# Kernel tuning notes

Hardware: AMD Instinct MI355X
Metric: run time of the kernel (lower is better)

Reference implementation:

```python
import jax, jax.numpy as jnp
import numpy as np

GRAY = 0.2989 + 0.5870 + 0.1140  # tf.image.rgb_to_grayscale weight sum (channels identical after grayscale_to_rgb)


def _resample(img, coords, axis):
    """Bilinear 1-D resample of `img` along `axis` at float `coords` (clamped)."""
    n = img.shape[axis]
    i0f = jnp.floor(coords)
    i0 = jnp.clip(i0f, 0, n - 1).astype(jnp.int32)
    i1 = jnp.clip(i0f + 1.0, 0, n - 1).astype(jnp.int32)
    f = coords - i0f
    a = jnp.take(img, i0, axis=axis)
    b = jnp.take(img, i1, axis=axis)
    shp = [1] * img.ndim
    shp[axis] = -1
    f = f.reshape(shp)
    return a * (1.0 - f) + b * f


def _aug_one(img, off_f, b, c, size, docrop, flp, k):
    S = img.shape[0]
    # ---- random crop (prob 0.5) + bilinear resize back to SxS (half-pixel centers) ----
    size_f = jnp.where(docrop, size.astype(jnp.float32), float(S))
    off = jnp.where(docrop, jnp.floor(off_f * (S - size_f + 1.0)), 0.0)  # [2] integer-valued offsets
    idx = (jnp.arange(S, dtype=jnp.float32) + 0.5) * (size_f / S) - 0.5
    img = _resample(img, idx + off[0], 0)
    img = _resample(img, idx + off[1], 1)
    # ---- random flip_left_right + rot90(k) ----
    img = jnp.where(flp, img[:, ::-1, :], img)
    rots = jnp.stack([img,
                      jnp.rot90(img, 1, (0, 1)),
                      jnp.rot90(img, 2, (0, 1)),
                      jnp.rot90(img, 3, (0, 1))])
    img = rots[k]
    # ---- per-channel brightness + contrast (gray->rgb->gray round trip == GRAY scale) ----
    x = img + b  # [S,S,C] + [C]
    m = jnp.mean(x, axis=(0, 1), keepdims=True)
    x = (x - m) * c + m
    return x * GRAY


def setup_inputs() -> dict:
    B, S, C = 64, 256, 5
    key = jax.random.key(0)
    ks = jax.random.split(key, 8)
    crops = jax.random.normal(ks[0], (B, S, S, C), dtype=jnp.float32)
    crop_size = jax.random.randint(ks[1], (B,), int(0.8 * S), S, dtype=jnp.int32)
    do_crop = jax.random.uniform(ks[2], (B,)) < 0.5
    off_frac = jax.random.uniform(ks[3], (B, 2), dtype=jnp.float32)
    flip = jax.random.uniform(ks[4], (B,)) < 0.5
    rot_k = jax.random.randint(ks[5], (B,), 0, 4, dtype=jnp.int32)
    bright = jax.random.uniform(ks[6], (B, C), minval=-0.1, maxval=0.1, dtype=jnp.float32)
    contrast = jax.random.uniform(ks[7], (B, C), minval=0.8, maxval=1.2, dtype=jnp.float32)
    return {"crops": crops, "off_frac": off_frac, "bright": bright, "contrast": contrast,
            "crop_size": crop_size, "do_crop": do_crop, "flip": flip, "rot_k": rot_k}


def reference(crops, off_frac, bright, contrast, crop_size, do_crop, flip, rot_k):
    return jax.vmap(_aug_one)(crops, off_frac, bright, contrast, crop_size, do_crop, flip, rot_k)
```

## Files before the change

kernel.cpp:

```cpp
#include <hip/hip_runtime.h>
#include <math.h>

#define SDIM 256
#define CH 5
#define ROWF (SDIM * CH)
#define NCHUNK 16
#define CHROWS 16
#define GRAYF 0.9999f

__global__ __launch_bounds__(256) void aug_sums_kernel(
    const float* __restrict__ crops,
    const float* __restrict__ off_frac,
    const int*   __restrict__ crop_size,
    const int*   __restrict__ do_crop,
    float* __restrict__ part)
{
    const int chunk = blockIdx.x;
    const int b     = blockIdx.y;
    const int tid   = threadIdx.x;

    __shared__ float wyl[SDIM];
    __shared__ float wxl[SDIM];
    __shared__ float psum[4][CH];

    const bool  docrop = do_crop[b] != 0;
    const float size_f = docrop ? (float)crop_size[b] : 256.0f;
    const float scale  = size_f * (1.0f / 256.0f);
    const float span   = 256.0f - size_f + 1.0f;
    const float off0   = docrop ? floorf(off_frac[2 * b + 0] * span) : 0.0f;
    const float off1   = docrop ? floorf(off_frac[2 * b + 1] * span) : 0.0f;

    wyl[tid] = 0.0f;
    wxl[tid] = 0.0f;
    __syncthreads();

    {
        const float cy = ((float)tid + 0.5f) * scale - 0.5f + off0;
        const float fl = floorf(cy);
        const float fy = cy - fl;
        const int r0 = min(max((int)fl, 0), 255);
        const int r1 = min(max((int)fl + 1, 0), 255);
        atomicAdd(&wyl[r0], 1.0f - fy);
        atomicAdd(&wyl[r1], fy);

        const float cx = ((float)tid + 0.5f) * scale - 0.5f + off1;
        const float fl2 = floorf(cx);
        const float fx  = cx - fl2;
        const int c0 = min(max((int)fl2, 0), 255);
        const int c1 = min(max((int)fl2 + 1, 0), 255);
        atomicAdd(&wxl[c0], 1.0f - fx);
        atomicAdd(&wxl[c1], fx);
    }
    __syncthreads();

    float accs[5] = {0.0f, 0.0f, 0.0f, 0.0f, 0.0f};

    const float4* src = reinterpret_cast<const float4*>(
        crops + ((size_t)b * SDIM + (size_t)chunk * CHROWS) * ROWF);
    for (int i = tid; i < CHROWS * 320; i += 256) {
        const int r    = i / 320;
        const int f4   = i - r * 320;
        const float4 v = src[i];
        const float  wr = wyl[chunk * CHROWS + r];
        const int base = f4 * 4;
        const int phase = base % 5;
        const float t0 = v.x * wxl[(base + 0) / 5] * wr;
        const float t1 = v.y * wxl[(base + 1) / 5] * wr;
        const float t2 = v.z * wxl[(base + 2) / 5] * wr;
        const float t3 = v.w * wxl[(base + 3) / 5] * wr;
        switch (phase) {
            case 0: accs[0]+=t0; accs[1]+=t1; accs[2]+=t2; accs[3]+=t3; break;
            case 1: accs[1]+=t0; accs[2]+=t1; accs[3]+=t2; accs[4]+=t3; break;
            case 2: accs[2]+=t0; accs[3]+=t1; accs[4]+=t2; accs[0]+=t3; break;
            case 3: accs[3]+=t0; accs[4]+=t1; accs[0]+=t2; accs[1]+=t3; break;
            default:accs[4]+=t0; accs[0]+=t1; accs[1]+=t2; accs[2]+=t3; break;
        }
    }

    const int lane = tid & 63;
    const int wv   = tid >> 6;
    #pragma unroll
    for (int ch = 0; ch < CH; ++ch) {
        float s = accs[ch];
        #pragma unroll
        for (int o = 32; o > 0; o >>= 1) s += __shfl_down(s, o, 64);
        if (lane == 0) psum[wv][ch] = s;
    }
    __syncthreads();
    if (tid == 0) {
        #pragma unroll
        for (int ch = 0; ch < CH; ++ch)
            part[((size_t)chunk * 64 + b) * CH + ch] =
                psum[0][ch] + psum[1][ch] + psum[2][ch] + psum[3][ch];
    }
}

__global__ __launch_bounds__(256) void aug_out_kernel(
    const float* __restrict__ crops,
    const float* __restrict__ off_frac,
    const int*   __restrict__ crop_size,
    const int*   __restrict__ do_crop,
    const int*   __restrict__ flip,
    const int*   __restrict__ rot_k,
    const float* __restrict__ part,
    const float* __restrict__ bright,
    const float* __restrict__ contrast,
    float* __restrict__ out)
{
    const int oi0 = blockIdx.x * 4;
    const int b   = blockIdx.y;
    const int tid = threadIdx.x;
    const int rr  = tid >> 6;
    const int xg  = tid & 63;

    __shared__ __align__(16) float smem[28 * 260];
    __shared__ float prm[2 * CH];

    const bool  docrop = do_crop[b] != 0;
    const float size_f = docrop ? (float)crop_size[b] : 256.0f;
    const float scale  = size_f * (1.0f / 256.0f);
    const float span   = 256.0f - size_f + 1.0f;
    const float off0   = docrop ? floorf(off_frac[2 * b + 0] * span) : 0.0f;
    const float off1   = docrop ? floorf(off_frac[2 * b + 1] * span) : 0.0f;
    const int   k      = rot_k[b] & 3;
    const bool  flp    = flip[b] != 0;

    if (tid < CH) {
        float s = 0.0f;
        #pragma unroll
        for (int p = 0; p < NCHUNK; ++p) s += part[((size_t)p * 64 + b) * CH + tid];
        const float m  = s * (1.0f / 65536.0f);
        const float co = contrast[b * CH + tid];
        const float br = bright[b * CH + tid];
        prm[tid]      = co * GRAYF;
        prm[CH + tid] = ((1.0f - co) * m + br) * GRAYF;
    }

    float vout[20];

    if ((k & 1) == 0) {
        const int y_min = (k == 0) ? oi0 : 255 - (oi0 + 3);
        const float cymin = ((float)y_min + 0.5f) * scale - 0.5f + off0;
        const int rbase = (int)floorf(cymin);

        const float4* src4 = reinterpret_cast<const float4*>(crops + (size_t)b * SDIM * ROWF);
        float4* dst4 = reinterpret_cast<float4*>(smem);
        for (int i = tid; i < 5 * 320; i += 256) {
            const int w  = i / 320;
            const int f4 = i - w * 320;
            const int rc = min(max(rbase + w, 0), 255);
            dst4[i] = src4[rc * 320 + f4];
        }
        __syncthreads();

        const int oi = oi0 + rr;
        const int y  = (k == 0) ? oi : 255 - oi;
        const float cy  = ((float)y + 0.5f) * scale - 0.5f + off0;
        const float flr = floorf(cy);
        const float fy  = cy - flr;
        const float* rbA = smem + ((int)flr - rbase) * ROWF;
        const float* rbB = rbA + ROWF;

        #pragma unroll
        for (int p = 0; p < 4; ++p) {
            const int oj = xg * 4 + p;
            const int xf = (k == 0) ? oj : 255 - oj;
            const int x  = flp ? 255 - xf : xf;
            const float cx  = ((float)x + 0.5f) * scale - 0.5f + off1;
            const float fl2 = floorf(cx);
            const float fx  = cx - fl2;
            const int c0 = min(max((int)fl2, 0), 255);
            const int c1 = min(max((int)fl2 + 1, 0), 255);
            #pragma unroll
            for (int ch = 0; ch < CH; ++ch) {
                const float aV = rbA[c0 * CH + ch] + fx * (rbA[c1 * CH + ch] - rbA[c0 * CH + ch]);
                const float dV = rbB[c0 * CH + ch] + fx * (rbB[c1 * CH + ch] - rbB[c0 * CH + ch]);
                vout[p * 5 + ch] = aV + fy * (dV - aV);
            }
        }
    } else {
        const int xfA = (k == 1) ? 255 - oi0 : oi0;
        const int xfB = (k == 1) ? 255 - (oi0 + 3) : oi0 + 3;
        const int xA = flp ? 255 - xfA : xfA;
        const int xB = flp ? 255 - xfB : xfB;
        const int xmin = min(xA, xB);
        const float cxmin = ((float)xmin + 0.5f) * scale - 0.5f + off1;
        const int cbase = (int)floorf(cxmin);
        const int basef = cbase * CH;
        const int base4 = basef & ~3;
        const bool fastp = (cbase >= 0) && (cbase + 4 <= 255) && (base4 >= 0) && (base4 + 28 <= ROWF);

        if (fastp) {
            const float4* rp = reinterpret_cast<const float4*>(
                crops + ((size_t)b * SDIM + tid) * ROWF + base4);
            const float4 q0 = rp[0], q1 = rp[1], q2 = rp[2], q3 = rp[3];
            const float4 q4 = rp[4], q5 = rp[5], q6 = rp[6];
            smem[ 0*260+tid]=q0.x; smem[ 1*260+tid]=q0.y; smem[ 2*260+tid]=q0.z; smem[ 3*260+tid]=q0.w;
            smem[ 4*260+tid]=q1.x; smem[ 5*260+tid]=q1.y; smem[ 6*260+tid]=q1.z; smem[ 7*260+tid]=q1.w;
            smem[ 8*260+tid]=q2.x; smem[ 9*260+tid]=q2.y; smem[10*260+tid]=q2.z; smem[11*260+tid]=q2.w;
            smem[12*260+tid]=q3.x; smem[13*260+tid]=q3.y; smem[14*260+tid]=q3.z; smem[15*260+tid]=q3.w;
            smem[16*260+tid]=q4.x; smem[17*260+tid]=q4.y; smem[18*260+tid]=q4.z; smem[19*260+tid]=q4.w;
            smem[20*260+tid]=q5.x; smem[21*260+tid]=q5.y; smem[22*260+tid]=q5.z; smem[23*260+tid]=q5.w;
            smem[24*260+tid]=q6.x; smem[25*260+tid]=q6.y; smem[26*260+tid]=q6.z; smem[27*260+tid]=q6.w;
        } else {
            #pragma unroll
            for (int w = 0; w < 28; ++w) {
                const int f2 = base4 + w + ROWF;
                const int c2 = f2 / 5;
                const int ch = f2 - c2 * 5;
                const int cc = min(max(c2 - 256, 0), 255);
                smem[w * 260 + tid] = crops[((size_t)b * SDIM + tid) * ROWF + cc * CH + ch];
            }
        }
        __syncthreads();

        const int oi = oi0 + rr;
        const int xf = (k == 1) ? 255 - oi : oi;
        const int x  = flp ? 255 - xf : xf;
        const float cx  = ((float)x + 0.5f) * scale - 0.5f + off1;
        const float fl2 = floorf(cx);
        const float fx  = cx - fl2;
        const int slotA = (int)fl2 * CH - base4;
        const int slotB = slotA + CH;

        #pragma unroll
        for (int p = 0; p < 4; ++p) {
            const int oj = xg * 4 + p;
            const int y  = (k == 1) ? oj : 255 - oj;
            const float cy  = ((float)y + 0.5f) * scale - 0.5f + off0;
            const float flr = floorf(cy);
            const float fy  = cy - flr;
            const int r0 = min(max((int)flr, 0), 255);
            const int r1 = min(max((int)flr + 1, 0), 255);
            #pragma unroll
            for (int ch = 0; ch < CH; ++ch) {
                const float p00 = smem[(slotA + ch) * 260 + r0];
                const float p01 = smem[(slotB + ch) * 260 + r0];
                const float p10 = smem[(slotA + ch) * 260 + r1];
                const float p11 = smem[(slotB + ch) * 260 + r1];
                const float aV = p00 + fx * (p01 - p00);
                const float dV = p10 + fx * (p11 - p10);
                vout[p * 5 + ch] = aV + fy * (dV - aV);
            }
        }
    }

    float aa[5], ab[5];
    #pragma unroll
    for (int ch = 0; ch < CH; ++ch) { aa[ch] = prm[ch]; ab[ch] = prm[CH + ch]; }

    float4* orow = reinterpret_cast<float4*>(out + ((size_t)b * SDIM + (oi0 + rr)) * ROWF);
    #pragma unroll
    for (int q = 0; q < 5; ++q) {
        float4 st;
        st.x = vout[q*4+0] * aa[(q*4+0)%5] + ab[(q*4+0)%5];
        st.y = vout[q*4+1] * aa[(q*4+1)%5] + ab[(q*4+1)%5];
        st.z = vout[q*4+2] * aa[(q*4+2)%5] + ab[(q*4+2)%5];
        st.w = vout[q*4+3] * aa[(q*4+3)%5] + ab[(q*4+3)%5];
        orow[xg * 5 + q] = st;
    }
}

extern "C" void kernel_launch(void* const* d_in, const int* in_sizes, int n_in,
                              void* d_out, int out_size, void* d_ws, size_t ws_size,
                              hipStream_t stream) {
    const float* crops     = (const float*)d_in[0];
    const float* off_frac  = (const float*)d_in[1];
    const float* bright    = (const float*)d_in[2];
    const float* contrast  = (const float*)d_in[3];
    const int*   crop_size = (const int*)d_in[4];
    const int*   do_crop   = (const int*)d_in[5];
    const int*   flipb     = (const int*)d_in[6];
    const int*   rot_k     = (const int*)d_in[7];

    float* out  = (float*)d_out;
    float* part = (float*)d_ws;

    dim3 blk(256);
    aug_sums_kernel<<<dim3(NCHUNK, 64), blk, 0, stream>>>(crops, off_frac, crop_size, do_crop, part);
    aug_out_kernel<<<dim3(SDIM / 4, 64), blk, 0, stream>>>(crops, off_frac, crop_size, do_crop,
                                                           flipb, rot_k, part, bright, contrast, out);
}
```

Measured before the change: 202.7 us.

## Stage output through LDS for coalesced stores; interleave column mapping; vectorize sums loop

The sums kernel now has each thread load five contiguous float4s covering four pixels and read their column weights as one float4. This replaces the per-element divide and modulo and the phase switch. The output kernel maps output columns with a lane stride of 64 instead of four consecutive columns per thread, which should cut LDS bank conflicts on the gather. Results are written to shared memory and then copied out as fully coalesced float4 rows. The cost is two extra barriers and an LDS round trip per block.

New measurement: 189.8 us. -6.4%, faster.

```diff
diff --git a/kernel.cpp b/kernel.cpp
--- a/kernel.cpp
+++ b/kernel.cpp
@@ -19,8 +19,8 @@
     const int b     = blockIdx.y;
     const int tid   = threadIdx.x;
 
-    __shared__ float wyl[SDIM];
-    __shared__ float wxl[SDIM];
+    __shared__ __align__(16) float wyl[SDIM];
+    __shared__ __align__(16) float wxl[SDIM];
     __shared__ float psum[4][CH];
 
     const bool  docrop = do_crop[b] != 0;
@@ -53,35 +53,32 @@
     }
     __syncthreads();
 
-    float accs[5] = {0.0f, 0.0f, 0.0f, 0.0f, 0.0f};
-
-    const float4* src = reinterpret_cast<const float4*>(
-        crops + ((size_t)b * SDIM + (size_t)chunk * CHROWS) * ROWF);
-    for (int i = tid; i < CHROWS * 320; i += 256) {
-        const int r    = i / 320;
-        const int f4   = i - r * 320;
-        const float4 v = src[i];
-        const float  wr = wyl[chunk * CHROWS + r];
-        const int base = f4 * 4;
-        const int phase = base % 5;
-        const float t0 = v.x * wxl[(base + 0) / 5] * wr;
-        const float t1 = v.y * wxl[(base + 1) / 5] * wr;
-        const float t2 = v.z * wxl[(base + 2) / 5] * wr;
-        const float t3 = v.w * wxl[(base + 3) / 5] * wr;
-        switch (phase) {
-            case 0: accs[0]+=t0; accs[1]+=t1; accs[2]+=t2; accs[3]+=t3; break;
-            case 1: accs[1]+=t0; accs[2]+=t1; accs[3]+=t2; accs[4]+=t3; break;
-            case 2: accs[2]+=t0; accs[3]+=t1; accs[4]+=t2; accs[0]+=t3; break;
-            case 3: accs[3]+=t0; accs[4]+=t1; accs[0]+=t2; accs[1]+=t3; break;
-            default:accs[4]+=t0; accs[0]+=t1; accs[1]+=t2; accs[2]+=t3; break;
-        }
+    float acc[5] = {0.0f, 0.0f, 0.0f, 0.0f, 0.0f};
+    const float* srcbase = crops + ((size_t)b * SDIM + (size_t)chunk * CHROWS) * ROWF;
+    const float4* wx4 = reinterpret_cast<const float4*>(wxl);
+
+    #pragma unroll
+    for (int it = 0; it < (CHROWS * 64) / 256; ++it) {
+        const int m = it * 256 + tid;
+        const int r = m >> 6;
+        const int t = m & 63;
+        const float4* p = reinterpret_cast<const float4*>(srcbase + r * ROWF + t * 20);
+        const float4 q0 = p[0], q1 = p[1], q2 = p[2], q3 = p[3], q4 = p[4];
+        const float wr = wyl[chunk * CHROWS + r];
+        const float4 wx = wx4[t];
+        const float w0 = wx.x * wr, w1 = wx.y * wr, w2 = wx.z * wr, w3 = wx.w * wr;
+        acc[0] += q0.x * w0; acc[1] += q0.y * w0; acc[2] += q0.z * w0; acc[3] += q0.w * w0;
+        acc[4] += q1.x * w0; acc[0] += q1.y * w1; acc[1] += q1.z * w1; acc[2] += q1.w * w1;
+        acc[3] += q2.x * w1; acc[4] += q2.y * w1; acc[0] += q2.z * w2; acc[1] += q2.w * w2;
+        acc[2] += q3.x * w2; acc[3] += q3.y * w2; acc[4] += q3.z * w2; acc[0] += q3.w * w3;
+        acc[1] += q4.x * w3; acc[2] += q4.y * w3; acc[3] += q4.z * w3; acc[4] += q4.w * w3;
     }
 
     const int lane = tid & 63;
     const int wv   = tid >> 6;
     #pragma unroll
     for (int ch = 0; ch < CH; ++ch) {
-        float s = accs[ch];
+        float s = acc[ch];
         #pragma unroll
         for (int o = 32; o > 0; o >>= 1) s += __shfl_down(s, o, 64);
         if (lane == 0) psum[wv][ch] = s;
@@ -107,11 +104,11 @@
     const float* __restrict__ contrast,
     float* __restrict__ out)
 {
-    const int oi0 = blockIdx.x * 4;
-    const int b   = blockIdx.y;
-    const int tid = threadIdx.x;
-    const int rr  = tid >> 6;
-    const int xg  = tid & 63;
+    const int oi0  = blockIdx.x * 4;
+    const int b    = blockIdx.y;
+    const int tid  = threadIdx.x;
+    const int rr   = tid >> 6;
+    const int lane = tid & 63;
 
     __shared__ __align__(16) float smem[28 * 260];
     __shared__ float prm[2 * CH];
@@ -163,7 +160,7 @@
 
         #pragma unroll
         for (int p = 0; p < 4; ++p) {
-            const int oj = xg * 4 + p;
+            const int oj = lane + 64 * p;
             const int xf = (k == 0) ? oj : 255 - oj;
             const int x  = flp ? 255 - xf : xf;
             const float cx  = ((float)x + 0.5f) * scale - 0.5f + off1;
@@ -186,8 +183,7 @@
         const int xmin = min(xA, xB);
         const float cxmin = ((float)xmin + 0.5f) * scale - 0.5f + off1;
         const int cbase = (int)floorf(cxmin);
-        const int basef = cbase * CH;
-        const int base4 = basef & ~3;
+        const int base4 = (cbase * CH) & ~3;
         const bool fastp = (cbase >= 0) && (cbase + 4 <= 255) && (base4 >= 0) && (base4 + 28 <= ROWF);
 
         if (fastp) {
@@ -225,7 +221,7 @@
 
         #pragma unroll
         for (int p = 0; p < 4; ++p) {
-            const int oj = xg * 4 + p;
+            const int oj = lane + 64 * p;
             const int y  = (k == 1) ? oj : 255 - oj;
             const float cy  = ((float)y + 0.5f) * scale - 0.5f + off0;
             const float flr = floorf(cy);
@@ -248,17 +244,26 @@
     float aa[5], ab[5];
     #pragma unroll
     for (int ch = 0; ch < CH; ++ch) { aa[ch] = prm[ch]; ab[ch] = prm[CH + ch]; }
-
-    float4* orow = reinterpret_cast<float4*>(out + ((size_t)b * SDIM + (oi0 + rr)) * ROWF);
-    #pragma unroll
-    for (int q = 0; q < 5; ++q) {
-        float4 st;
-        st.x = vout[q*4+0] * aa[(q*4+0)%5] + ab[(q*4+0)%5];
-        st.y = vout[q*4+1] * aa[(q*4+1)%5] + ab[(q*4+1)%5];
-        st.z = vout[q*4+2] * aa[(q*4+2)%5] + ab[(q*4+2)%5];
-        st.w = vout[q*4+3] * aa[(q*4+3)%5] + ab[(q*4+3)%5];
-        orow[xg * 5 + q] = st;
-    }
+    #pragma unroll
+    for (int p = 0; p < 4; ++p)
+        #pragma unroll
+        for (int ch = 0; ch < CH; ++ch)
+            vout[p * 5 + ch] = vout[p * 5 + ch] * aa[ch] + ab[ch];
+
+    __syncthreads();
+    #pragma unroll
+    for (int p = 0; p < 4; ++p) {
+        const int oj = lane + 64 * p;
+        #pragma unroll
+        for (int ch = 0; ch < CH; ++ch)
+            smem[rr * ROWF + oj * CH + ch] = vout[p * 5 + ch];
+    }
+    __syncthreads();
+
+    const float4* ob4 = reinterpret_cast<const float4*>(smem);
+    float4* dst = reinterpret_cast<float4*>(out + ((size_t)b * SDIM + oi0) * ROWF);
+    #pragma unroll
+    for (int q = 0; q < 5; ++q) dst[q * 256 + tid] = ob4[q * 256 + tid];
 }
 
 extern "C" void kernel_launch(void* const* d_in, const int* in_sizes, int n_in,
```
